# Kernel optimization log

Measured on AMD Instinct MI355X. Metric: run time of the kernel, lower is better.

The kernel has to match this reference:

```python
import jax, jax.numpy as jnp
import numpy as np

NB = 2        # trm_num_blocks
H = 4         # trm_num_heads
D = 128       # trm_hidden_dim
L = 512
B = 1
PAD = 0
NEG = jnp.float32(-2**32 + 1)


def _ln(x, g, b, eps=1e-8):
    m = x.mean(-1, keepdims=True)
    v = x.var(-1, keepdims=True)
    return (x - m) / jnp.sqrt(v + eps) * g + b


def setup_inputs() -> dict:
    key = jax.random.key(0)
    ks = jax.random.split(key, 16)
    s = 0.02
    inp = {
        "log_seqs": jax.random.randint(ks[0], (B, L), 0, 1000),
        "seqs": jax.random.normal(ks[1], (B, L, D), jnp.float32),
        "time_matrix_K": jax.random.normal(ks[2], (B, L, L, D), jnp.float32),
        # per-block stacked params [NB, ...]
        "Wq": jax.random.normal(ks[3], (NB, D, D), jnp.float32) * s,
        "bq": jnp.zeros((NB, D), jnp.float32),
        "Wk": jax.random.normal(ks[4], (NB, D, D), jnp.float32) * s,
        "bk": jnp.zeros((NB, D), jnp.float32),
        "Wv": jax.random.normal(ks[5], (NB, D, D), jnp.float32) * s,
        "bv": jnp.zeros((NB, D), jnp.float32),
        "Wt": jax.random.normal(ks[6], (NB, D, D), jnp.float32) * s,
        "bt": jnp.zeros((NB, D), jnp.float32),
        "Wtp": jax.random.normal(ks[7], (NB, D, 1), jnp.float32) * s,
        "btp": jnp.zeros((NB, 1), jnp.float32),
        "ln1_g": jnp.ones((NB, D), jnp.float32),
        "ln1_b": jnp.zeros((NB, D), jnp.float32),
        "ln2_g": jnp.ones((NB, D), jnp.float32),
        "ln2_b": jnp.zeros((NB, D), jnp.float32),
        "W1": jax.random.normal(ks[8], (NB, D, D), jnp.float32) * s,
        "b1": jnp.zeros((NB, D), jnp.float32),
        "W2": jax.random.normal(ks[9], (NB, D, D), jnp.float32) * s,
        "b2": jnp.zeros((NB, D), jnp.float32),
        "lnf_g": jnp.ones((D,), jnp.float32),
        "lnf_b": jnp.zeros((D,), jnp.float32),
    }
    return inp


def reference(log_seqs, seqs, time_matrix_K, Wq, bq, Wk, bk, Wv, bv, Wt, bt,
              Wtp, btp, ln1_g, ln1_b, ln2_g, ln2_b, W1, b1, W2, b2, lnf_g, lnf_b):
    hd = D // H
    pad = (log_seqs == PAD)                     # [B, L] True at padding
    keep = (~pad)[..., None].astype(seqs.dtype)  # [B, L, 1]
    seqs = seqs * keep
    causal = ~jnp.tril(jnp.ones((L, L), bool))  # True above diagonal (masked)
    # combined mask [1, B, L, L]: pad query rows OR non-causal entries
    mask = pad[None, :, :, None] | causal[None, None, :, :]

    attn_ws = []
    for i in range(NB):
        Q = _ln(seqs, ln1_g[i], ln1_b[i])
        q = Q @ Wq[i] + bq[i]
        k = seqs @ Wk[i] + bk[i]
        v = seqs @ Wv[i] + bv[i]
        # head-major layout [H, B, L, hd] (matches torch split+cat along dim 0)
        qh = q.reshape(B, L, H, hd).transpose(2, 0, 1, 3)
        kh = k.reshape(B, L, H, hd).transpose(2, 0, 1, 3)
        vh = v.reshape(B, L, H, hd).transpose(2, 0, 1, 3)
        scores = jnp.einsum('hbqd,hbkd->hbqk', qh, kh)  # [H, B, L, L]
        # time bias: sigmoid(proj(relu(W_t t))) in (0,1); log is negative
        tw = jax.nn.sigmoid(
            (jax.nn.relu(time_matrix_K @ Wt[i] + bt[i]) @ Wtp[i] + btp[i]).squeeze(-1)
        )                                             # [B, L, L]
        scores = (scores + jnp.log(tw)) / jnp.float32(hd) ** 0.5
        scores = jnp.where(mask, NEG, scores)
        w = jax.nn.softmax(scores, axis=-1)           # dropout is identity (eval)
        attn_ws.append(w.reshape(H * B, L, L))
        out = jnp.einsum('hbqk,hbkd->hbqd', w, vh).transpose(1, 2, 0, 3).reshape(B, L, D)
        seqs = Q + out
        x = _ln(seqs, ln2_g[i], ln2_b[i])
        y = jax.nn.relu(x @ W1[i] + b1[i]) @ W2[i] + b2[i]
        seqs = (x + y) * keep                         # FFN residual adds post-LN x
    log_feats = _ln(seqs, lnf_g, lnf_b)
    return (log_feats, tuple(attn_ws))
```

## Files before the change

### kernel.cpp

```cpp
#include <hip/hip_runtime.h>

#define L 512
#define D 128
#define H 4
#define HD 32

typedef __bf16 bf16x8 __attribute__((ext_vector_type(8)));
typedef float  f32x4  __attribute__((ext_vector_type(4)));

__device__ __forceinline__ float wave_sum(float v){
#pragma unroll
  for (int o = 32; o; o >>= 1) v += __shfl_xor(v, o);
  return v;
}
__device__ __forceinline__ unsigned short bfbits(float v){
  __bf16 h = (__bf16)v;
  unsigned short u;
  __builtin_memcpy(&u, &h, 2);
  return u;
}

__global__ void k_bfrag(const float* __restrict__ Wt, unsigned short* __restrict__ bf){
  int idx = blockIdx.x * 256 + threadIdx.x;
  int jj   = idx & 7;
  int lane = (idx >> 3) & 63;
  int k0   = (idx >> 9) & 3;
  int nt   = idx >> 11;
  int d    = k0 * 32 + (lane >> 4) * 8 + jj;
  int col  = (nt & 7) * 16 + (lane & 15);
  int blk  = nt >> 3;
  bf[idx] = bfbits(Wt[blk * D * D + d * D + col]);
}

__global__ __launch_bounds__(256, 2) void k_timebias(
    const float* __restrict__ T, const unsigned short* __restrict__ bfg,
    const float* __restrict__ bt, const float* __restrict__ wtp,
    const float* __restrict__ btp, float* __restrict__ logtw){
  __shared__ __align__(16) unsigned short bsh[32768];
  __shared__ float bts[256], wtps[256];
  int tid = threadIdx.x;
  {
    const uint4* g = (const uint4*)bfg;
    uint4* s = (uint4*)bsh;
#pragma unroll
    for (int i = 0; i < 16; ++i) s[tid + i * 256] = g[tid + i * 256];
    bts[tid]  = bt[tid];
    wtps[tid] = wtp[tid];
  }
  __syncthreads();

  int lane = tid & 63, w = tid >> 6;
  int quad = lane >> 4, m = lane & 15;
  const bf16x8* bls = (const bf16x8*)bsh;
  int wbase = blockIdx.x * 256 + w * 64;

  bf16x8 afr[4][4];
#pragma unroll
  for (int mt = 0; mt < 4; ++mt){
    const float* tp = T + (size_t)(wbase + mt * 16 + m) * D + quad * 8;
#pragma unroll
    for (int k0 = 0; k0 < 4; ++k0){
      float4 f0 = *(const float4*)(tp + k0 * 32);
      float4 f1 = *(const float4*)(tp + k0 * 32 + 4);
      bf16x8 a;
      a[0] = (__bf16)f0.x; a[1] = (__bf16)f0.y; a[2] = (__bf16)f0.z; a[3] = (__bf16)f0.w;
      a[4] = (__bf16)f1.x; a[5] = (__bf16)f1.y; a[6] = (__bf16)f1.z; a[7] = (__bf16)f1.w;
      afr[mt][k0] = a;
    }
  }

#pragma unroll
  for (int blk = 0; blk < 2; ++blk){
    f32x4 rs[4] = {{0,0,0,0},{0,0,0,0},{0,0,0,0},{0,0,0,0}};
#pragma unroll
    for (int ntl = 0; ntl < 8; ++ntl){
      int nt = blk * 8 + ntl;
      f32x4 acc[4] = {{0,0,0,0},{0,0,0,0},{0,0,0,0},{0,0,0,0}};
#pragma unroll
      for (int k0 = 0; k0 < 4; ++k0){
        bf16x8 b = bls[(nt * 4 + k0) * 64 + lane];
#pragma unroll
        for (int mt = 0; mt < 4; ++mt)
          acc[mt] = __builtin_amdgcn_mfma_f32_16x16x32_bf16(afr[mt][k0], b, acc[mt], 0, 0, 0);
      }
      float btv = bts[nt * 16 + m];
      float wtv = wtps[nt * 16 + m];
#pragma unroll
      for (int mt = 0; mt < 4; ++mt)
#pragma unroll
        for (int r = 0; r < 4; ++r)
          rs[mt][r] += fmaxf(acc[mt][r] + btv, 0.f) * wtv;
    }
#pragma unroll
    for (int mt = 0; mt < 4; ++mt)
#pragma unroll
      for (int r = 0; r < 4; ++r){
        float v = rs[mt][r];
        v += __shfl_xor(v, 1); v += __shfl_xor(v, 2);
        v += __shfl_xor(v, 4); v += __shfl_xor(v, 8);
        rs[mt][r] = v;
      }
    if (m == 0){
      float bp = btp[blk];
      float* out = logtw + blk * (L * L);
#pragma unroll
      for (int mt = 0; mt < 4; ++mt){
        float4 o;
        float s0 = rs[mt][0] + bp; o.x = -logf(1.f + expf(-s0));
        float s1 = rs[mt][1] + bp; o.y = -logf(1.f + expf(-s1));
        float s2 = rs[mt][2] + bp; o.z = -logf(1.f + expf(-s2));
        float s3 = rs[mt][3] + bp; o.w = -logf(1.f + expf(-s3));
        *(float4*)(out + wbase + mt * 16 + quad * 4) = o;
      }
    }
  }
}

__device__ __forceinline__ void write_qA(unsigned short* qA, int row, int c, float v){
  int qt = row >> 4, m = row & 15;
  int h = c >> 5, cc = c & 31;
  qA[(((qt * 4 + h) * 64) + (cc >> 3) * 16 + m) * 8 + (cc & 7)] = bfbits(v);
}
__device__ __forceinline__ void write_kB(unsigned short* kB, int row, int c, float v){
  int h = c >> 5, cc = c & 31;
  int nt = row >> 4;
  kB[((h * 32 + nt) * 64 + (cc >> 3) * 16 + (row & 15)) * 8 + (cc & 7)] = bfbits(v);
}
__device__ __forceinline__ void write_vB(unsigned short* vB, int row, int c, float v){
  int h = c >> 5, cc = c & 31;
  int kk = row >> 5, qv = (row >> 3) & 3, jv = row & 7;
  int nt = cc >> 4;
  vB[(((h * 16 + kk) * 2 + nt) * 64 + qv * 16 + (cc & 15)) * 8 + jv] = bfbits(v);
}

__global__ __launch_bounds__(128) void k_qkv0(
    const float* __restrict__ src, const int* __restrict__ ls,
    const float* __restrict__ g1, const float* __restrict__ b1,
    const float* __restrict__ Wq, const float* __restrict__ bq,
    const float* __restrict__ Wk, const float* __restrict__ bk,
    const float* __restrict__ Wv, const float* __restrict__ bv,
    float* __restrict__ Q, unsigned short* __restrict__ qA,
    unsigned short* __restrict__ kB, unsigned short* __restrict__ vB){
  __shared__ float xs[128], Qs[128], tmp[2];
  int row = blockIdx.x, c = threadIdx.x;
  float xv = src[row * D + c];
  if (ls[row] == 0) xv = 0.f;
  float s = wave_sum(xv);
  if ((c & 63) == 0) tmp[c >> 6] = s;
  __syncthreads();
  float mean = (tmp[0] + tmp[1]) * (1.f / 128.f);
  __syncthreads();
  float dv = xv - mean;
  float s2 = wave_sum(dv * dv);
  if ((c & 63) == 0) tmp[c >> 6] = s2;
  __syncthreads();
  float var = fmaxf((tmp[0] + tmp[1]) * (1.f / 128.f), 0.f);
  float qn = dv * rsqrtf(var + 1e-8f) * g1[c] + b1[c];
  xs[c] = xv; Qs[c] = qn;
  Q[row * D + c] = qn;
  __syncthreads();
  float aq = 0.f, ak = 0.f, av = 0.f;
#pragma unroll 4
  for (int k = 0; k < 128; ++k){
    float xq = Qs[k], xk = xs[k];
    aq += xq * Wq[k * D + c];
    ak += xk * Wk[k * D + c];
    av += xk * Wv[k * D + c];
  }
  write_qA(qA, row, c, aq + bq[c]);
  write_kB(kB, row, c, ak + bk[c]);
  write_vB(vB, row, c, av + bv[c]);
}

__global__ __launch_bounds__(256) void k_attn(
    const unsigned short* __restrict__ qA, const unsigned short* __restrict__ kB,
    const unsigned short* __restrict__ vB, const float* __restrict__ logtw,
    const int* __restrict__ ls, const float* __restrict__ Q,
    float* __restrict__ wout, float* __restrict__ xr){
  __shared__ __align__(16) unsigned short pa[16 * 64 * 8];
  __shared__ float pvp[4][2][64][4];
  __shared__ float smax[4][16], ssum[4][16];
  int qt = blockIdx.x >> 2, h = blockIdx.x & 3;
  int tid = threadIdx.x, lane = tid & 63, w = tid >> 6;
  int quad = lane >> 4, mcol = lane & 15;
  const float RS = 0.17677669529663687f;

  bf16x8 qf = ((const bf16x8*)qA)[(qt * 4 + h) * 64 + lane];

  f32x4 acc[8];
#pragma unroll
  for (int nt8 = 0; nt8 < 8; ++nt8){
    bf16x8 bf = ((const bf16x8*)kB)[(h * 32 + w * 8 + nt8) * 64 + lane];
    f32x4 z = {0, 0, 0, 0};
    acc[nt8] = __builtin_amdgcn_mfma_f32_16x16x32_bf16(qf, bf, z, 0, 0, 0);
  }

  float e[8][4];
  float mx4[4] = {-3e38f, -3e38f, -3e38f, -3e38f};
#pragma unroll
  for (int nt8 = 0; nt8 < 8; ++nt8){
    int col = w * 128 + nt8 * 16 + mcol;
#pragma unroll
    for (int r = 0; r < 4; ++r){
      int row = qt * 16 + quad * 4 + r;
      float sv = (acc[nt8][r] + logtw[row * L + col]) * RS;
      sv = (col <= row) ? sv : -3e38f;
      e[nt8][r] = sv;
      mx4[r] = fmaxf(mx4[r], sv);
    }
  }
#pragma unroll
  for (int r = 0; r < 4; ++r){
    float v = mx4[r];
    v = fmaxf(v, __shfl_xor(v, 1)); v = fmaxf(v, __shfl_xor(v, 2));
    v = fmaxf(v, __shfl_xor(v, 4)); v = fmaxf(v, __shfl_xor(v, 8));
    mx4[r] = v;
  }
  if (mcol == 0){
#pragma unroll
    for (int r = 0; r < 4; ++r) smax[w][quad * 4 + r] = mx4[r];
  }
  __syncthreads();
  float mxr[4], sum4[4] = {0, 0, 0, 0};
#pragma unroll
  for (int r = 0; r < 4; ++r){
    int rr = quad * 4 + r;
    mxr[r] = fmaxf(fmaxf(smax[0][rr], smax[1][rr]), fmaxf(smax[2][rr], smax[3][rr]));
  }
#pragma unroll
  for (int nt8 = 0; nt8 < 8; ++nt8)
#pragma unroll
    for (int r = 0; r < 4; ++r){
      float sv = e[nt8][r];
      float ev = (sv > -1e38f) ? expf(sv - mxr[r]) : 0.f;
      e[nt8][r] = ev;
      sum4[r] += ev;
    }
#pragma unroll
  for (int r = 0; r < 4; ++r){
    float v = sum4[r];
    v += __shfl_xor(v, 1); v += __shfl_xor(v, 2);
    v += __shfl_xor(v, 4); v += __shfl_xor(v, 8);
    sum4[r] = v;
  }
  if (mcol == 0){
#pragma unroll
    for (int r = 0; r < 4; ++r) ssum[w][quad * 4 + r] = sum4[r];
  }
  __syncthreads();
  float inv[4]; int padr[4];
#pragma unroll
  for (int r = 0; r < 4; ++r){
    int rr = quad * 4 + r;
    inv[r] = 1.f / (ssum[0][rr] + ssum[1][rr] + ssum[2][rr] + ssum[3][rr]);
    padr[r] = (ls[qt * 16 + rr] == 0);
  }
#pragma unroll
  for (int nt8 = 0; nt8 < 8; ++nt8){
    int col = w * 128 + nt8 * 16 + mcol;
    int kk = col >> 5, qk = (col >> 3) & 3, jj = col & 7;
#pragma unroll
    for (int r = 0; r < 4; ++r){
      int rl = quad * 4 + r;
      float wv = padr[r] ? (1.f / 512.f) : e[nt8][r] * inv[r];
      wout[h * (L * L) + (qt * 16 + rl) * L + col] = wv;
      pa[(kk * 64 + qk * 16 + rl) * 8 + jj] = bfbits(wv);
    }
  }

  f32x4 pacc[2] = {{0,0,0,0},{0,0,0,0}};
#pragma unroll
  for (int kk4 = 0; kk4 < 4; ++kk4){
    int kk = w * 4 + kk4;
    bf16x8 af = ((const bf16x8*)pa)[kk * 64 + lane];
#pragma unroll
    for (int nt = 0; nt < 2; ++nt){
      bf16x8 bf = ((const bf16x8*)vB)[((h * 16 + kk) * 2 + nt) * 64 + lane];
      pacc[nt] = __builtin_amdgcn_mfma_f32_16x16x32_bf16(af, bf, pacc[nt], 0, 0, 0);
    }
  }
#pragma unroll
  for (int nt = 0; nt < 2; ++nt)
#pragma unroll
    for (int r = 0; r < 4; ++r) pvp[w][nt][lane][r] = pacc[nt][r];
  __syncthreads();
  if (w < 2){
    int nt = w;
#pragma unroll
    for (int r = 0; r < 4; ++r){
      float o = pvp[0][nt][lane][r] + pvp[1][nt][lane][r]
              + pvp[2][nt][lane][r] + pvp[3][nt][lane][r];
      int row = qt * 16 + quad * 4 + r;
      int cg = h * HD + nt * 16 + mcol;
      xr[row * D + cg] = Q[row * D + cg] + o;
    }
  }
}

__global__ __launch_bounds__(256) void k_ffn(
    const float* __restrict__ xr, const int* __restrict__ ls,
    const float* __restrict__ g2, const float* __restrict__ b2,
    const float* __restrict__ W1, const float* __restrict__ b1f,
    const float* __restrict__ W2, const float* __restrict__ b2f,
    int fuse_qkv,
    const float* __restrict__ g1, const float* __restrict__ b1,
    const float* __restrict__ Wq, const float* __restrict__ bq,
    const float* __restrict__ Wk, const float* __restrict__ bk,
    const float* __restrict__ Wv, const float* __restrict__ bv,
    float* __restrict__ Q, unsigned short* __restrict__ qA,
    unsigned short* __restrict__ kB, unsigned short* __restrict__ vB,
    int fuse_lnf, const float* __restrict__ lg, const float* __restrict__ lb,
    float* __restrict__ lf){
  __shared__ float xrs[128], x2s[128], y1s[128], pstore[256], st[2];
  int row = blockIdx.x, tid = threadIdx.x;
  int c = tid & 127, half = tid >> 7;
  if (half == 0) xrs[c] = xr[row * D + c];
  __syncthreads();
  if (tid < 64){
    float a = xrs[tid], b = xrs[tid + 64];
    float s1 = wave_sum(a + b);
    float s2 = wave_sum(a * a + b * b);
    if (tid == 0){
      float mean = s1 * (1.f / 128.f);
      float var = fmaxf(s2 * (1.f / 128.f) - mean * mean, 0.f);
      st[0] = mean; st[1] = rsqrtf(var + 1e-8f);
    }
  }
  __syncthreads();
  if (half == 0) x2s[c] = (xrs[c] - st[0]) * st[1] * g2[c] + b2[c];
  __syncthreads();
  float a1 = 0.f;
  { int k0 = half * 64;
#pragma unroll 8
    for (int k = 0; k < 64; ++k) a1 += x2s[k0 + k] * W1[(k0 + k) * D + c]; }
  pstore[tid] = a1;
  __syncthreads();
  if (half == 0) y1s[c] = fmaxf(pstore[c] + pstore[c + 128] + b1f[c], 0.f);
  __syncthreads();
  float a2 = 0.f;
  { int k0 = half * 64;
#pragma unroll 8
    for (int k = 0; k < 64; ++k) a2 += y1s[k0 + k] * W2[(k0 + k) * D + c]; }
  pstore[tid] = a2;
  __syncthreads();
  float kp = (ls[row] != 0) ? 1.f : 0.f;
  if (half == 0)
    xrs[c] = (x2s[c] + pstore[c] + pstore[c + 128] + b2f[c]) * kp;
  __syncthreads();

  if (fuse_qkv){
    if (tid < 64){
      float a = xrs[tid], b = xrs[tid + 64];
      float s1 = wave_sum(a + b);
      float s2 = wave_sum(a * a + b * b);
      if (tid == 0){
        float mean = s1 * (1.f / 128.f);
        float var = fmaxf(s2 * (1.f / 128.f) - mean * mean, 0.f);
        st[0] = mean; st[1] = rsqrtf(var + 1e-8f);
      }
    }
    __syncthreads();
    if (half == 0){
      float qn = (xrs[c] - st[0]) * st[1] * g1[c] + b1[c];
      y1s[c] = qn;
      Q[row * D + c] = qn;
    }
    __syncthreads();
    float avp = 0.f;
    if (half == 0){
      float aq = 0.f;
#pragma unroll 4
      for (int k = 0; k < 128; ++k) aq += y1s[k] * Wq[k * D + c];
#pragma unroll 8
      for (int k = 0; k < 64; ++k) avp += xrs[k] * Wv[k * D + c];
      write_qA(qA, row, c, aq + bq[c]);
    } else {
      float ak = 0.f;
#pragma unroll 4
      for (int k = 0; k < 128; ++k) ak += xrs[k] * Wk[k * D + c];
#pragma unroll 8
      for (int k = 64; k < 128; ++k) avp += xrs[k] * Wv[k * D + c];
      write_kB(kB, row, c, ak + bk[c]);
    }
    pstore[tid] = avp;
    __syncthreads();
    if (half == 1)
      write_vB(vB, row, c, pstore[c] + pstore[c + 128] + bv[c]);
  }

  if (fuse_lnf){
    if (tid < 64){
      float a = xrs[tid], b = xrs[tid + 64];
      float s1 = wave_sum(a + b);
      float s2 = wave_sum(a * a + b * b);
      if (tid == 0){
        float mean = s1 * (1.f / 128.f);
        float var = fmaxf(s2 * (1.f / 128.f) - mean * mean, 0.f);
        st[0] = mean; st[1] = rsqrtf(var + 1e-8f);
      }
    }
    __syncthreads();
    if (half == 0) lf[row * D + c] = (xrs[c] - st[0]) * st[1] * lg[c] + lb[c];
  }
}

extern "C" void kernel_launch(void* const* d_in, const int* in_sizes, int n_in,
                              void* d_out, int out_size, void* d_ws, size_t ws_size,
                              hipStream_t stream){
  const int*   ls   = (const int*)d_in[0];
  const float* seqs = (const float*)d_in[1];
  const float* T    = (const float*)d_in[2];
  const float* Wq   = (const float*)d_in[3];
  const float* bq   = (const float*)d_in[4];
  const float* Wk   = (const float*)d_in[5];
  const float* bk   = (const float*)d_in[6];
  const float* Wv   = (const float*)d_in[7];
  const float* bv   = (const float*)d_in[8];
  const float* Wt   = (const float*)d_in[9];
  const float* bt   = (const float*)d_in[10];
  const float* Wtp  = (const float*)d_in[11];
  const float* btp  = (const float*)d_in[12];
  const float* g1   = (const float*)d_in[13];
  const float* b1   = (const float*)d_in[14];
  const float* g2   = (const float*)d_in[15];
  const float* b2   = (const float*)d_in[16];
  const float* W1   = (const float*)d_in[17];
  const float* b1f  = (const float*)d_in[18];
  const float* W2   = (const float*)d_in[19];
  const float* b2f  = (const float*)d_in[20];
  const float* lg   = (const float*)d_in[21];
  const float* lb   = (const float*)d_in[22];

  float* ws    = (float*)d_ws;
  float* Q     = ws;
  float* xr    = Q + 65536;
  float* logtw = xr + 65536;
  unsigned short* bfg = (unsigned short*)(logtw + 2 * 262144);
  unsigned short* qA  = bfg + 32768;
  unsigned short* kB  = qA + 65536;
  unsigned short* vB  = kB + 65536;

  float* outF = (float*)d_out;
  float* lf = outF;
  float* w0 = outF + 65536;
  float* w1 = w0 + 1048576;

  k_bfrag   <<<128, 256, 0, stream>>>(Wt, bfg);
  k_timebias<<<1024, 256, 0, stream>>>(T, bfg, bt, Wtp, btp, logtw);

  k_qkv0<<<512, 128, 0, stream>>>(seqs, ls, g1, b1, Wq, bq, Wk, bk, Wv, bv,
                                  Q, qA, kB, vB);
  k_attn<<<128, 256, 0, stream>>>(qA, kB, vB, logtw, ls, Q, w0, xr);
  k_ffn<<<512, 256, 0, stream>>>(xr, ls, g2, b2, W1, b1f, W2, b2f,
                                 1, g1 + D, b1 + D, Wq + D * D, bq + D,
                                 Wk + D * D, bk + D, Wv + D * D, bv + D,
                                 Q, qA, kB, vB,
                                 0, lg, lb, lf);
  k_attn<<<128, 256, 0, stream>>>(qA, kB, vB, logtw + L * L, ls, Q, w1, xr);
  k_ffn<<<512, 256, 0, stream>>>(xr, ls, g2 + D, b2 + D, W1 + D * D, b1f + D,
                                 W2 + D * D, b2f + D,
                                 0, g1, b1, Wq, bq, Wk, bk, Wv, bv,
                                 Q, qA, kB, vB,
                                 1, lg, lb, lf);
}
```

Measured before the change: 321.0 us.

## Move QKV and FFN projections to bf16 MFMA over 16-row tiles

Replaces the per-row scalar FP32 QKV and FFN matvec kernels with 16-row tile kernels that use bf16 MFMA. All projection weights are pre-converted into fragment layout by a single prep kernel. The timebias kernel now stages Wt one block at a time, halving its LDS so more workgroups can be resident (launch bounds raised to 4). The risk is lower precision in the projections, and these launches now use only 32 workgroups.

```diff
diff --git a/kernel.cpp b/kernel.cpp
--- a/kernel.cpp
+++ b/kernel.cpp
@@ -4,51 +4,120 @@
 #define D 128
 #define H 4
 #define HD 32
+#define XLD 132
 
 typedef __bf16 bf16x8 __attribute__((ext_vector_type(8)));
 typedef float  f32x4  __attribute__((ext_vector_type(4)));
 
-__device__ __forceinline__ float wave_sum(float v){
-#pragma unroll
-  for (int o = 32; o; o >>= 1) v += __shfl_xor(v, o);
-  return v;
-}
 __device__ __forceinline__ unsigned short bfbits(float v){
-  __bf16 h = (__bf16)v;
-  unsigned short u;
-  __builtin_memcpy(&u, &h, 2);
-  return u;
-}
-
-__global__ void k_bfrag(const float* __restrict__ Wt, unsigned short* __restrict__ bf){
+  __bf16 h = (__bf16)v; unsigned short u; __builtin_memcpy(&u, &h, 2); return u;
+}
+__device__ __forceinline__ bf16x8 cvt8(float4 a0, float4 a1){
+  bf16x8 r;
+  r[0] = (__bf16)a0.x; r[1] = (__bf16)a0.y; r[2] = (__bf16)a0.z; r[3] = (__bf16)a0.w;
+  r[4] = (__bf16)a1.x; r[5] = (__bf16)a1.y; r[6] = (__bf16)a1.z; r[7] = (__bf16)a1.w;
+  return r;
+}
+
+__device__ __forceinline__ void write_qA(unsigned short* qA, int row, int c, float v){
+  int qt = row >> 4, m = row & 15;
+  int h = c >> 5, cc = c & 31;
+  qA[(((qt * 4 + h) * 64) + (cc >> 3) * 16 + m) * 8 + (cc & 7)] = bfbits(v);
+}
+__device__ __forceinline__ void write_kB(unsigned short* kB, int row, int c, float v){
+  int h = c >> 5, cc = c & 31;
+  int nt = row >> 4;
+  kB[((h * 32 + nt) * 64 + (cc >> 3) * 16 + (row & 15)) * 8 + (cc & 7)] = bfbits(v);
+}
+__device__ __forceinline__ void write_vB(unsigned short* vB, int row, int c, float v){
+  int h = c >> 5, cc = c & 31;
+  int kk = row >> 5, qv = (row >> 3) & 3, jv = row & 7;
+  int nt = cc >> 4;
+  vB[(((h * 16 + kk) * 2 + nt) * 64 + qv * 16 + (cc & 15)) * 8 + jv] = bfbits(v);
+}
+
+__device__ __forceinline__ void row_stats16(const float (*buf)[XLD], int tid,
+                                            float* mean_s, float* rstd_s){
+  int row_l = tid >> 4, seg = tid & 15;
+  const float* p = &buf[row_l][seg * 8];
+  float4 f0 = *(const float4*)p, f1 = *(const float4*)(p + 4);
+  float sum = f0.x + f0.y + f0.z + f0.w + f1.x + f1.y + f1.z + f1.w;
+  float sq  = f0.x*f0.x + f0.y*f0.y + f0.z*f0.z + f0.w*f0.w
+            + f1.x*f1.x + f1.y*f1.y + f1.z*f1.z + f1.w*f1.w;
+#pragma unroll
+  for (int o = 1; o < 16; o <<= 1){ sum += __shfl_xor(sum, o); sq += __shfl_xor(sq, o); }
+  if (seg == 0){
+    float mn = sum * (1.f / 128.f);
+    mean_s[row_l] = mn;
+    rstd_s[row_l] = rsqrtf(fmaxf(sq * (1.f / 128.f) - mn * mn, 0.f) + 1e-8f);
+  }
+}
+
+__device__ __forceinline__ void build_afr(const float (*buf)[XLD], int lane, bf16x8* afr){
+  int m = lane & 15, quad = lane >> 4;
+#pragma unroll
+  for (int k0 = 0; k0 < 4; ++k0){
+    const float* p = &buf[m][k0 * 32 + quad * 8];
+    afr[k0] = cvt8(*(const float4*)p, *(const float4*)(p + 4));
+  }
+}
+__device__ __forceinline__ void build_afr_ln(const float (*buf)[XLD], int lane,
+    const float* mean_s, const float* rstd_s,
+    const float* __restrict__ g, const float* __restrict__ b, bf16x8* afr){
+  int m = lane & 15, quad = lane >> 4;
+  float mn = mean_s[m], rs = rstd_s[m];
+#pragma unroll
+  for (int k0 = 0; k0 < 4; ++k0){
+    int c0 = k0 * 32 + quad * 8;
+    const float* p = &buf[m][c0];
+    float4 a0 = *(const float4*)p, a1 = *(const float4*)(p + 4);
+    float q[8];
+    q[0]=(a0.x-mn)*rs*g[c0+0]+b[c0+0]; q[1]=(a0.y-mn)*rs*g[c0+1]+b[c0+1];
+    q[2]=(a0.z-mn)*rs*g[c0+2]+b[c0+2]; q[3]=(a0.w-mn)*rs*g[c0+3]+b[c0+3];
+    q[4]=(a1.x-mn)*rs*g[c0+4]+b[c0+4]; q[5]=(a1.y-mn)*rs*g[c0+5]+b[c0+5];
+    q[6]=(a1.z-mn)*rs*g[c0+6]+b[c0+6]; q[7]=(a1.w-mn)*rs*g[c0+7]+b[c0+7];
+    bf16x8 r;
+    r[0]=(__bf16)q[0]; r[1]=(__bf16)q[1]; r[2]=(__bf16)q[2]; r[3]=(__bf16)q[3];
+    r[4]=(__bf16)q[4]; r[5]=(__bf16)q[5]; r[6]=(__bf16)q[6]; r[7]=(__bf16)q[7];
+    afr[k0] = r;
+  }
+}
+
+__global__ void k_prep(const float* __restrict__ Wt,
+                       const float* __restrict__ Wq, const float* __restrict__ Wk,
+                       const float* __restrict__ Wv, const float* __restrict__ W1,
+                       const float* __restrict__ W2,
+                       unsigned short* __restrict__ bfg, unsigned short* __restrict__ wf){
   int idx = blockIdx.x * 256 + threadIdx.x;
-  int jj   = idx & 7;
-  int lane = (idx >> 3) & 63;
-  int k0   = (idx >> 9) & 3;
-  int nt   = idx >> 11;
-  int d    = k0 * 32 + (lane >> 4) * 8 + jj;
-  int col  = (nt & 7) * 16 + (lane & 15);
-  int blk  = nt >> 3;
-  bf[idx] = bfbits(Wt[blk * D * D + d * D + col]);
-}
-
-__global__ __launch_bounds__(256, 2) void k_timebias(
+  if (idx < 32768){
+    int jj   = idx & 7;
+    int lane = (idx >> 3) & 63;
+    int k0   = (idx >> 9) & 3;
+    int nt   = idx >> 11;
+    int d    = k0 * 32 + (lane >> 4) * 8 + jj;
+    int col  = (nt & 7) * 16 + (lane & 15);
+    int blk  = nt >> 3;
+    bfg[idx] = bfbits(Wt[blk * D * D + d * D + col]);
+  } else {
+    int i2 = idx - 32768;
+    int jj = i2 & 7, lane = (i2 >> 3) & 63, k0 = (i2 >> 9) & 3, nt = (i2 >> 11) & 7;
+    int mat = i2 >> 14;
+    int blk = mat / 5, m5 = mat % 5;
+    const float* W = (m5 == 0 ? Wq : m5 == 1 ? Wk : m5 == 2 ? Wv : m5 == 3 ? W1 : W2)
+                     + blk * D * D;
+    int d = k0 * 32 + (lane >> 4) * 8 + jj;
+    int col = nt * 16 + (lane & 15);
+    wf[i2] = bfbits(W[d * D + col]);
+  }
+}
+
+__global__ __launch_bounds__(256, 4) void k_timebias(
     const float* __restrict__ T, const unsigned short* __restrict__ bfg,
     const float* __restrict__ bt, const float* __restrict__ wtp,
     const float* __restrict__ btp, float* __restrict__ logtw){
-  __shared__ __align__(16) unsigned short bsh[32768];
-  __shared__ float bts[256], wtps[256];
+  __shared__ __align__(16) unsigned short bsh[16384];
+  __shared__ float bts[128], wtps[128];
   int tid = threadIdx.x;
-  {
-    const uint4* g = (const uint4*)bfg;
-    uint4* s = (uint4*)bsh;
-#pragma unroll
-    for (int i = 0; i < 16; ++i) s[tid + i * 256] = g[tid + i * 256];
-    bts[tid]  = bt[tid];
-    wtps[tid] = wtp[tid];
-  }
-  __syncthreads();
-
   int lane = tid & 63, w = tid >> 6;
   int quad = lane >> 4, m = lane & 15;
   const bf16x8* bls = (const bf16x8*)bsh;
@@ -62,29 +131,35 @@
     for (int k0 = 0; k0 < 4; ++k0){
       float4 f0 = *(const float4*)(tp + k0 * 32);
       float4 f1 = *(const float4*)(tp + k0 * 32 + 4);
-      bf16x8 a;
-      a[0] = (__bf16)f0.x; a[1] = (__bf16)f0.y; a[2] = (__bf16)f0.z; a[3] = (__bf16)f0.w;
-      a[4] = (__bf16)f1.x; a[5] = (__bf16)f1.y; a[6] = (__bf16)f1.z; a[7] = (__bf16)f1.w;
-      afr[mt][k0] = a;
+      afr[mt][k0] = cvt8(f0, f1);
     }
   }
 
 #pragma unroll
   for (int blk = 0; blk < 2; ++blk){
+    if (blk) __syncthreads();
+    {
+      const uint4* g = (const uint4*)(bfg + blk * 16384);
+      uint4* s = (uint4*)bsh;
+#pragma unroll
+      for (int i = 0; i < 8; ++i) s[tid + i * 256] = g[tid + i * 256];
+      if (tid < 128){ bts[tid] = bt[blk * 128 + tid]; wtps[tid] = wtp[blk * 128 + tid]; }
+    }
+    __syncthreads();
+
     f32x4 rs[4] = {{0,0,0,0},{0,0,0,0},{0,0,0,0},{0,0,0,0}};
 #pragma unroll
     for (int ntl = 0; ntl < 8; ++ntl){
-      int nt = blk * 8 + ntl;
       f32x4 acc[4] = {{0,0,0,0},{0,0,0,0},{0,0,0,0},{0,0,0,0}};
 #pragma unroll
       for (int k0 = 0; k0 < 4; ++k0){
-        bf16x8 b = bls[(nt * 4 + k0) * 64 + lane];
+        bf16x8 b = bls[(ntl * 4 + k0) * 64 + lane];
 #pragma unroll
         for (int mt = 0; mt < 4; ++mt)
           acc[mt] = __builtin_amdgcn_mfma_f32_16x16x32_bf16(afr[mt][k0], b, acc[mt], 0, 0, 0);
       }
-      float btv = bts[nt * 16 + m];
-      float wtv = wtps[nt * 16 + m];
+      float btv = bts[ntl * 16 + m];
+      float wtv = wtps[ntl * 16 + m];
 #pragma unroll
       for (int mt = 0; mt < 4; ++mt)
 #pragma unroll
@@ -116,60 +191,71 @@
   }
 }
 
-__device__ __forceinline__ void write_qA(unsigned short* qA, int row, int c, float v){
-  int qt = row >> 4, m = row & 15;
-  int h = c >> 5, cc = c & 31;
-  qA[(((qt * 4 + h) * 64) + (cc >> 3) * 16 + m) * 8 + (cc & 7)] = bfbits(v);
-}
-__device__ __forceinline__ void write_kB(unsigned short* kB, int row, int c, float v){
-  int h = c >> 5, cc = c & 31;
-  int nt = row >> 4;
-  kB[((h * 32 + nt) * 64 + (cc >> 3) * 16 + (row & 15)) * 8 + (cc & 7)] = bfbits(v);
-}
-__device__ __forceinline__ void write_vB(unsigned short* vB, int row, int c, float v){
-  int h = c >> 5, cc = c & 31;
-  int kk = row >> 5, qv = (row >> 3) & 3, jv = row & 7;
-  int nt = cc >> 4;
-  vB[(((h * 16 + kk) * 2 + nt) * 64 + qv * 16 + (cc & 15)) * 8 + jv] = bfbits(v);
-}
-
-__global__ __launch_bounds__(128) void k_qkv0(
-    const float* __restrict__ src, const int* __restrict__ ls,
+__global__ __launch_bounds__(256) void k_qkv_m(
+    const float* __restrict__ src, const int* __restrict__ ls, int domask,
     const float* __restrict__ g1, const float* __restrict__ b1,
-    const float* __restrict__ Wq, const float* __restrict__ bq,
-    const float* __restrict__ Wk, const float* __restrict__ bk,
-    const float* __restrict__ Wv, const float* __restrict__ bv,
+    const unsigned short* __restrict__ wf, int matq,
+    const float* __restrict__ bq, const float* __restrict__ bk,
+    const float* __restrict__ bv,
     float* __restrict__ Q, unsigned short* __restrict__ qA,
     unsigned short* __restrict__ kB, unsigned short* __restrict__ vB){
-  __shared__ float xs[128], Qs[128], tmp[2];
-  int row = blockIdx.x, c = threadIdx.x;
-  float xv = src[row * D + c];
-  if (ls[row] == 0) xv = 0.f;
-  float s = wave_sum(xv);
-  if ((c & 63) == 0) tmp[c >> 6] = s;
-  __syncthreads();
-  float mean = (tmp[0] + tmp[1]) * (1.f / 128.f);
-  __syncthreads();
-  float dv = xv - mean;
-  float s2 = wave_sum(dv * dv);
-  if ((c & 63) == 0) tmp[c >> 6] = s2;
-  __syncthreads();
-  float var = fmaxf((tmp[0] + tmp[1]) * (1.f / 128.f), 0.f);
-  float qn = dv * rsqrtf(var + 1e-8f) * g1[c] + b1[c];
-  xs[c] = xv; Qs[c] = qn;
-  Q[row * D + c] = qn;
-  __syncthreads();
-  float aq = 0.f, ak = 0.f, av = 0.f;
-#pragma unroll 4
-  for (int k = 0; k < 128; ++k){
-    float xq = Qs[k], xk = xs[k];
-    aq += xq * Wq[k * D + c];
-    ak += xk * Wk[k * D + c];
-    av += xk * Wv[k * D + c];
-  }
-  write_qA(qA, row, c, aq + bq[c]);
-  write_kB(kB, row, c, ak + bk[c]);
-  write_vB(vB, row, c, av + bv[c]);
+  __shared__ float xs[16][XLD];
+  __shared__ float mean_s[16], rstd_s[16];
+  __shared__ float g1s[128], b1s[128];
+  int tid = threadIdx.x, rowbase = blockIdx.x * 16;
+  int row_l = tid >> 4, seg = tid & 15;
+
+  const float* sp = src + (rowbase + row_l) * D + seg * 8;
+  float4 f0 = *(const float4*)sp, f1 = *(const float4*)(sp + 4);
+  if (domask && ls[rowbase + row_l] == 0){
+    f0 = make_float4(0,0,0,0); f1 = make_float4(0,0,0,0);
+  }
+  *(float4*)&xs[row_l][seg * 8] = f0;
+  *(float4*)&xs[row_l][seg * 8 + 4] = f1;
+  if (tid < 128){ g1s[tid] = g1[tid]; b1s[tid] = b1[tid]; }
+  __syncthreads();
+  row_stats16(xs, tid, mean_s, rstd_s);
+  __syncthreads();
+
+  {
+    float mn = mean_s[row_l], rs = rstd_s[row_l];
+    float* qp = Q + (rowbase + row_l) * D + seg * 8;
+    float4 o0, o1;
+    int c0 = seg * 8;
+    o0.x=(f0.x-mn)*rs*g1s[c0+0]+b1s[c0+0]; o0.y=(f0.y-mn)*rs*g1s[c0+1]+b1s[c0+1];
+    o0.z=(f0.z-mn)*rs*g1s[c0+2]+b1s[c0+2]; o0.w=(f0.w-mn)*rs*g1s[c0+3]+b1s[c0+3];
+    o1.x=(f1.x-mn)*rs*g1s[c0+4]+b1s[c0+4]; o1.y=(f1.y-mn)*rs*g1s[c0+5]+b1s[c0+5];
+    o1.z=(f1.z-mn)*rs*g1s[c0+6]+b1s[c0+6]; o1.w=(f1.w-mn)*rs*g1s[c0+7]+b1s[c0+7];
+    *(float4*)qp = o0; *(float4*)(qp + 4) = o1;
+  }
+
+  int lane = tid & 63, w = tid >> 6;
+  int quad = lane >> 4, mcol = lane & 15;
+  bf16x8 afrQ[4], afrX[4];
+  build_afr_ln(xs, lane, mean_s, rstd_s, g1s, b1s, afrQ);
+  build_afr(xs, lane, afrX);
+
+#pragma unroll
+  for (int jl = 0; jl < 6; ++jl){
+    int j = w * 6 + jl;
+    int mat = j >> 3, nt = j & 7;
+    const bf16x8* wfb = (const bf16x8*)wf + ((size_t)(matq + mat) * 8 + nt) * 4 * 64;
+    f32x4 acc = {0, 0, 0, 0};
+#pragma unroll
+    for (int k0 = 0; k0 < 4; ++k0)
+      acc = __builtin_amdgcn_mfma_f32_16x16x32_bf16(mat == 0 ? afrQ[k0] : afrX[k0],
+                                                    wfb[k0 * 64 + lane], acc, 0, 0, 0);
+    int c = nt * 16 + mcol;
+    float bias = (mat == 0 ? bq : mat == 1 ? bk : bv)[c];
+#pragma unroll
+    for (int r = 0; r < 4; ++r){
+      int row = rowbase + quad * 4 + r;
+      float v = acc[r] + bias;
+      if (mat == 0) write_qA(qA, row, c, v);
+      else if (mat == 1) write_kB(kB, row, c, v);
+      else write_vB(vB, row, c, v);
+    }
+  }
 }
 
 __global__ __launch_bounds__(256) void k_attn(
@@ -297,110 +383,148 @@
   }
 }
 
-__global__ __launch_bounds__(256) void k_ffn(
+__global__ __launch_bounds__(256) void k_ffn_m(
     const float* __restrict__ xr, const int* __restrict__ ls,
     const float* __restrict__ g2, const float* __restrict__ b2,
-    const float* __restrict__ W1, const float* __restrict__ b1f,
-    const float* __restrict__ W2, const float* __restrict__ b2f,
-    int fuse_qkv,
-    const float* __restrict__ g1, const float* __restrict__ b1,
-    const float* __restrict__ Wq, const float* __restrict__ bq,
-    const float* __restrict__ Wk, const float* __restrict__ bk,
-    const float* __restrict__ Wv, const float* __restrict__ bv,
+    const unsigned short* __restrict__ wf, int mat1,
+    const float* __restrict__ b1f, const float* __restrict__ b2f,
+    int fuse_qkv, const float* __restrict__ g1, const float* __restrict__ b1,
+    int matq, const float* __restrict__ bq, const float* __restrict__ bk,
+    const float* __restrict__ bv,
     float* __restrict__ Q, unsigned short* __restrict__ qA,
     unsigned short* __restrict__ kB, unsigned short* __restrict__ vB,
     int fuse_lnf, const float* __restrict__ lg, const float* __restrict__ lb,
     float* __restrict__ lf){
-  __shared__ float xrs[128], x2s[128], y1s[128], pstore[256], st[2];
-  int row = blockIdx.x, tid = threadIdx.x;
-  int c = tid & 127, half = tid >> 7;
-  if (half == 0) xrs[c] = xr[row * D + c];
-  __syncthreads();
-  if (tid < 64){
-    float a = xrs[tid], b = xrs[tid + 64];
-    float s1 = wave_sum(a + b);
-    float s2 = wave_sum(a * a + b * b);
-    if (tid == 0){
-      float mean = s1 * (1.f / 128.f);
-      float var = fmaxf(s2 * (1.f / 128.f) - mean * mean, 0.f);
-      st[0] = mean; st[1] = rsqrtf(var + 1e-8f);
-    }
-  }
-  __syncthreads();
-  if (half == 0) x2s[c] = (xrs[c] - st[0]) * st[1] * g2[c] + b2[c];
-  __syncthreads();
-  float a1 = 0.f;
-  { int k0 = half * 64;
-#pragma unroll 8
-    for (int k = 0; k < 64; ++k) a1 += x2s[k0 + k] * W1[(k0 + k) * D + c]; }
-  pstore[tid] = a1;
-  __syncthreads();
-  if (half == 0) y1s[c] = fmaxf(pstore[c] + pstore[c + 128] + b1f[c], 0.f);
-  __syncthreads();
-  float a2 = 0.f;
-  { int k0 = half * 64;
-#pragma unroll 8
-    for (int k = 0; k < 64; ++k) a2 += y1s[k0 + k] * W2[(k0 + k) * D + c]; }
-  pstore[tid] = a2;
-  __syncthreads();
-  float kp = (ls[row] != 0) ? 1.f : 0.f;
-  if (half == 0)
-    xrs[c] = (x2s[c] + pstore[c] + pstore[c + 128] + b2f[c]) * kp;
+  __shared__ float xs[16][XLD];
+  __shared__ float x2s[16][XLD];
+  __shared__ float y1s[16][XLD];
+  __shared__ float xos[16][XLD];
+  __shared__ float mean_s[16], rstd_s[16];
+  __shared__ float gs[128], bs[128];
+  int tid = threadIdx.x, rowbase = blockIdx.x * 16;
+  int row_l = tid >> 4, seg = tid & 15;
+  int lane = tid & 63, w = tid >> 6;
+  int quad = lane >> 4, mcol = lane & 15;
+
+  {
+    const float* sp = xr + (rowbase + row_l) * D + seg * 8;
+    *(float4*)&xs[row_l][seg * 8] = *(const float4*)sp;
+    *(float4*)&xs[row_l][seg * 8 + 4] = *(const float4*)(sp + 4);
+    if (tid < 128){ gs[tid] = g2[tid]; bs[tid] = b2[tid]; }
+  }
+  __syncthreads();
+  row_stats16(xs, tid, mean_s, rstd_s);
+  __syncthreads();
+  {
+    float mn = mean_s[row_l], rs = rstd_s[row_l];
+#pragma unroll
+    for (int i = 0; i < 8; ++i){
+      int c = seg * 8 + i;
+      x2s[row_l][c] = (xs[row_l][c] - mn) * rs * gs[c] + bs[c];
+    }
+  }
+  __syncthreads();
+
+  bf16x8 afr[4];
+  build_afr(x2s, lane, afr);
+#pragma unroll
+  for (int jl = 0; jl < 2; ++jl){
+    int nt = w * 2 + jl;
+    const bf16x8* wfb = (const bf16x8*)wf + ((size_t)mat1 * 8 + nt) * 4 * 64;
+    f32x4 acc = {0, 0, 0, 0};
+#pragma unroll
+    for (int k0 = 0; k0 < 4; ++k0)
+      acc = __builtin_amdgcn_mfma_f32_16x16x32_bf16(afr[k0], wfb[k0 * 64 + lane], acc, 0, 0, 0);
+    int c = nt * 16 + mcol;
+    float bias = b1f[c];
+#pragma unroll
+    for (int r = 0; r < 4; ++r)
+      y1s[quad * 4 + r][c] = fmaxf(acc[r] + bias, 0.f);
+  }
+  __syncthreads();
+
+  build_afr(y1s, lane, afr);
+#pragma unroll
+  for (int jl = 0; jl < 2; ++jl){
+    int nt = w * 2 + jl;
+    const bf16x8* wfb = (const bf16x8*)wf + ((size_t)(mat1 + 1) * 8 + nt) * 4 * 64;
+    f32x4 acc = {0, 0, 0, 0};
+#pragma unroll
+    for (int k0 = 0; k0 < 4; ++k0)
+      acc = __builtin_amdgcn_mfma_f32_16x16x32_bf16(afr[k0], wfb[k0 * 64 + lane], acc, 0, 0, 0);
+    int c = nt * 16 + mcol;
+    float bias = b2f[c];
+#pragma unroll
+    for (int r = 0; r < 4; ++r){
+      int rl = quad * 4 + r;
+      float kp = (ls[rowbase + rl] != 0) ? 1.f : 0.f;
+      xos[rl][c] = (x2s[rl][c] + acc[r] + bias) * kp;
+    }
+  }
   __syncthreads();
 
   if (fuse_qkv){
-    if (tid < 64){
-      float a = xrs[tid], b = xrs[tid + 64];
-      float s1 = wave_sum(a + b);
-      float s2 = wave_sum(a * a + b * b);
-      if (tid == 0){
-        float mean = s1 * (1.f / 128.f);
-        float var = fmaxf(s2 * (1.f / 128.f) - mean * mean, 0.f);
-        st[0] = mean; st[1] = rsqrtf(var + 1e-8f);
+    if (tid < 128){ gs[tid] = g1[tid]; bs[tid] = b1[tid]; }
+    row_stats16(xos, tid, mean_s, rstd_s);
+    __syncthreads();
+    {
+      float mn = mean_s[row_l], rs = rstd_s[row_l];
+      float* qp = Q + (rowbase + row_l) * D + seg * 8;
+      float4 o0, o1;
+      int c0 = seg * 8;
+      o0.x=(xos[row_l][c0+0]-mn)*rs*gs[c0+0]+bs[c0+0];
+      o0.y=(xos[row_l][c0+1]-mn)*rs*gs[c0+1]+bs[c0+1];
+      o0.z=(xos[row_l][c0+2]-mn)*rs*gs[c0+2]+bs[c0+2];
+      o0.w=(xos[row_l][c0+3]-mn)*rs*gs[c0+3]+bs[c0+3];
+      o1.x=(xos[row_l][c0+4]-mn)*rs*gs[c0+4]+bs[c0+4];
+      o1.y=(xos[row_l][c0+5]-mn)*rs*gs[c0+5]+bs[c0+5];
+      o1.z=(xos[row_l][c0+6]-mn)*rs*gs[c0+6]+bs[c0+6];
+      o1.w=(xos[row_l][c0+7]-mn)*rs*gs[c0+7]+bs[c0+7];
+      *(float4*)qp = o0; *(float4*)(qp + 4) = o1;
+    }
+    bf16x8 afrQ[4], afrX[4];
+    build_afr_ln(xos, lane, mean_s, rstd_s, gs, bs, afrQ);
+    build_afr(xos, lane, afrX);
+#pragma unroll
+    for (int jl = 0; jl < 6; ++jl){
+      int j = w * 6 + jl;
+      int mat = j >> 3, nt = j & 7;
+      const bf16x8* wfb = (const bf16x8*)wf + ((size_t)(matq + mat) * 8 + nt) * 4 * 64;
+      f32x4 acc = {0, 0, 0, 0};
+#pragma unroll
+      for (int k0 = 0; k0 < 4; ++k0)
+        acc = __builtin_amdgcn_mfma_f32_16x16x32_bf16(mat == 0 ? afrQ[k0] : afrX[k0],
+                                                      wfb[k0 * 64 + lane], acc, 0, 0, 0);
+      int c = nt * 16 + mcol;
+      float bias = (mat == 0 ? bq : mat == 1 ? bk : bv)[c];
+#pragma unroll
+      for (int r = 0; r < 4; ++r){
+        int row = rowbase + quad * 4 + r;
+        float v = acc[r] + bias;
+        if (mat == 0) write_qA(qA, row, c, v);
+        else if (mat == 1) write_kB(kB, row, c, v);
+        else write_vB(vB, row, c, v);
       }
     }
+  }
+
+  if (fuse_lnf){
+    if (tid < 128){ gs[tid] = lg[tid]; bs[tid] = lb[tid]; }
+    row_stats16(xos, tid, mean_s, rstd_s);
     __syncthreads();
-    if (half == 0){
-      float qn = (xrs[c] - st[0]) * st[1] * g1[c] + b1[c];
-      y1s[c] = qn;
-      Q[row * D + c] = qn;
-    }
-    __syncthreads();
-    float avp = 0.f;
-    if (half == 0){
-      float aq = 0.f;
-#pragma unroll 4
-      for (int k = 0; k < 128; ++k) aq += y1s[k] * Wq[k * D + c];
-#pragma unroll 8
-      for (int k = 0; k < 64; ++k) avp += xrs[k] * Wv[k * D + c];
-      write_qA(qA, row, c, aq + bq[c]);
-    } else {
-      float ak = 0.f;
-#pragma unroll 4
-      for (int k = 0; k < 128; ++k) ak += xrs[k] * Wk[k * D + c];
-#pragma unroll 8
-      for (int k = 64; k < 128; ++k) avp += xrs[k] * Wv[k * D + c];
-      write_kB(kB, row, c, ak + bk[c]);
-    }
-    pstore[tid] = avp;
-    __syncthreads();
-    if (half == 1)
-      write_vB(vB, row, c, pstore[c] + pstore[c + 128] + bv[c]);
-  }
-
-  if (fuse_lnf){
-    if (tid < 64){
-      float a = xrs[tid], b = xrs[tid + 64];
-      float s1 = wave_sum(a + b);
-      float s2 = wave_sum(a * a + b * b);
-      if (tid == 0){
-        float mean = s1 * (1.f / 128.f);
-        float var = fmaxf(s2 * (1.f / 128.f) - mean * mean, 0.f);
-        st[0] = mean; st[1] = rsqrtf(var + 1e-8f);
-      }
-    }
-    __syncthreads();
-    if (half == 0) lf[row * D + c] = (xrs[c] - st[0]) * st[1] * lg[c] + lb[c];
+    float mn = mean_s[row_l], rs = rstd_s[row_l];
+    float* op = lf + (rowbase + row_l) * D + seg * 8;
+    float4 o0, o1;
+    int c0 = seg * 8;
+    o0.x=(xos[row_l][c0+0]-mn)*rs*gs[c0+0]+bs[c0+0];
+    o0.y=(xos[row_l][c0+1]-mn)*rs*gs[c0+1]+bs[c0+1];
+    o0.z=(xos[row_l][c0+2]-mn)*rs*gs[c0+2]+bs[c0+2];
+    o0.w=(xos[row_l][c0+3]-mn)*rs*gs[c0+3]+bs[c0+3];
+    o1.x=(xos[row_l][c0+4]-mn)*rs*gs[c0+4]+bs[c0+4];
+    o1.y=(xos[row_l][c0+5]-mn)*rs*gs[c0+5]+bs[c0+5];
+    o1.z=(xos[row_l][c0+6]-mn)*rs*gs[c0+6]+bs[c0+6];
+    o1.w=(xos[row_l][c0+7]-mn)*rs*gs[c0+7]+bs[c0+7];
+    *(float4*)op = o0; *(float4*)(op + 4) = o1;
   }
 }
 
@@ -436,7 +560,8 @@
   float* xr    = Q + 65536;
   float* logtw = xr + 65536;
   unsigned short* bfg = (unsigned short*)(logtw + 2 * 262144);
-  unsigned short* qA  = bfg + 32768;
+  unsigned short* wf  = bfg + 32768;
+  unsigned short* qA  = wf + 163840;
   unsigned short* kB  = qA + 65536;
   unsigned short* vB  = kB + 65536;
 
@@ -445,21 +570,19 @@
   float* w0 = outF + 65536;
   float* w1 = w0 + 1048576;
 
-  k_bfrag   <<<128, 256, 0, stream>>>(Wt, bfg);
+  k_prep    <<<768, 256, 0, stream>>>(Wt, Wq, Wk, Wv, W1, W2, bfg, wf);
   k_timebias<<<1024, 256, 0, stream>>>(T, bfg, bt, Wtp, btp, logtw);
 
-  k_qkv0<<<512, 128, 0, stream>>>(seqs, ls, g1, b1, Wq, bq, Wk, bk, Wv, bv,
+  k_qkv_m<<<32, 256, 0, stream>>>(seqs, ls, 1, g1, b1, wf, 0, bq, bk, bv,
                                   Q, qA, kB, vB);
   k_attn<<<128, 256, 0, stream>>>(qA, kB, vB, logtw, ls, Q, w0, xr);
-  k_ffn<<<512, 256, 0, stream>>>(xr, ls, g2, b2, W1, b1f, W2, b2f,
-                                 1, g1 + D, b1 + D, Wq + D * D, bq + D,
-                                 Wk + D * D, bk + D, Wv + D * D, bv + D,
-                                 Q, qA, kB, vB,
-                                 0, lg, lb, lf);
+  k_ffn_m<<<32, 256, 0, stream>>>(xr, ls, g2, b2, wf, 3, b1f, b2f,
+                                  1, g1 + D, b1 + D, 5, bq + D, bk + D, bv + D,
+                                  Q, qA, kB, vB,
+                                  0, lg, lb, lf);
   k_attn<<<128, 256, 0, stream>>>(qA, kB, vB, logtw + L * L, ls, Q, w1, xr);
-  k_ffn<<<512, 256, 0, stream>>>(xr, ls, g2 + D, b2 + D, W1 + D * D, b1f + D,
-                                 W2 + D * D, b2f + D,
-                                 0, g1, b1, Wq, bq, Wk, bk, Wv, bv,
-                                 Q, qA, kB, vB,
-                                 1, lg, lb, lf);
-}
+  k_ffn_m<<<32, 256, 0, stream>>>(xr, ls, g2 + D, b2 + D, wf, 8, b1f + D, b2f + D,
+                                  0, g1, b1, 0, bq, bk, bv,
+                                  Q, qA, kB, vB,
+                                  1, lg, lb, lf);
+}
```

Result: faster. 299.1 us (-6.8%).
